# Optimization experiments

Hardware: AMD Instinct MI355X
Metric: run time of the kernel (lower is better)

## Reference

```python
import jax, jax.numpy as jnp
import numpy as np

EPSILON = 1e-8
K = 3  # three-nearest-neighbor interpolation


def setup_inputs() -> dict:
    key = jax.random.key(0)
    k1, k2, k3 = jax.random.split(key, 3)
    B, N1, N2, C = 8, 1024, 4096, 256
    p1 = jax.random.normal(k1, (B, N1, 3), dtype=jnp.float32)  # coarse coords
    x1 = jax.random.normal(k2, (B, C, N1), dtype=jnp.float32)  # coarse features (channel-first)
    p2 = jax.random.normal(k3, (B, N2, 3), dtype=jnp.float32)  # fine coords
    return {"p1": p1, "x1": x1, "p2": p2}


def reference(p1, x1, p2):
    # Squared pairwise distances [B, N2, N1] via the expansion trick.
    d2 = (
        jnp.sum(p2 * p2, axis=-1, keepdims=True)
        - 2.0 * jnp.einsum("bmd,bnd->bmn", p2, p1)
        + jnp.sum(p1 * p1, axis=-1)[:, None, :]
    )
    # K smallest distances (pointops.nearestneighbor returns squared dists).
    neg_top, idx = jax.lax.top_k(-d2, K)  # [B, N2, K]
    dist = -neg_top
    # Reciprocal-distance weights, normalized over the K neighbors.
    dist_recip = 1.0 / (dist + EPSILON)
    weight = dist_recip / jnp.sum(dist_recip, axis=-1, keepdims=True)  # [B, N2, K]
    # Gather neighbor features and blend: up_x1[b,c,m] = sum_k w[b,m,k] * x1[b,c,idx[b,m,k]]
    x1t = jnp.swapaxes(x1, 1, 2)  # [B, N1, C]
    gathered = jax.vmap(lambda f, i: f[i])(x1t, idx)  # [B, N2, K, C]
    up_x1 = jnp.einsum("bmkc,bmk->bcm", gathered, weight)  # [B, C, N2]
    return up_x1
```

## Files before the change

### kernel.cpp

```cpp
#include <hip/hip_runtime.h>
#include <cfloat>
#include <climits>

#define B_   8
#define N1_  1024
#define N2_  4096
#define C_   256
#define TPQ  16
#define QPB  (256 / TPQ)

__device__ __forceinline__ unsigned umin_(unsigned a, unsigned b) { return a < b ? a : b; }

__device__ __forceinline__ unsigned umed3_(unsigned a, unsigned b, unsigned c) {
    unsigned d;
    asm("v_med3_u32 %0, %1, %2, %3" : "=v"(d) : "v"(a), "v"(b), "v"(c));
    return d;
}

#define KINS4(k, k0, k1, k2, k3) do {                 \
    unsigned _n1 = umed3_((k), k0, k1);               \
    unsigned _n2 = umed3_((k), k1, k2);               \
    unsigned _n3 = umed3_((k), k2, k3);               \
    k0 = umin_((k), k0);  k1 = _n1;  k2 = _n2;  k3 = _n3; \
} while (0)

__global__ __launch_bounds__(256) void knn_kernel(
    const float* __restrict__ p1, const float* __restrict__ p2,
    int4* __restrict__ wsi, float4* __restrict__ wsw) {
    __shared__ float4 pts[N1_];

    const int tid   = threadIdx.x;
    const int b     = blockIdx.x >> 8;
    const int mtile = blockIdx.x & 255;

    for (int j = tid; j < N1_; j += 256) {
        float x = p1[((size_t)b * N1_ + j) * 3 + 0];
        float y = p1[((size_t)b * N1_ + j) * 3 + 1];
        float z = p1[((size_t)b * N1_ + j) * 3 + 2];
        float s1 = __fadd_rn(__fadd_rn(__fmul_rn(x, x), __fmul_rn(y, y)),
                             __fmul_rn(z, z));
        pts[j] = make_float4(x + x, y + y, z + z, s1);
    }
    __syncthreads();

    const int q = tid >> 4;
    const int t = tid & 15;
    const int m = mtile * QPB + q;

    const size_t pbase = ((size_t)b * N2_ + m) * 3;
    const float x2 = p2[pbase + 0];
    const float y2 = p2[pbase + 1];
    const float z2 = p2[pbase + 2];
    const float s2 = __fadd_rn(__fadd_rn(__fmul_rn(x2, x2), __fmul_rn(y2, y2)),
                               __fmul_rn(z2, z2));

    unsigned k0 = UINT_MAX, k1 = UINT_MAX, k2 = UINT_MAX, k3 = UINT_MAX;

#pragma unroll 4
    for (int n = t; n < N1_; n += TPQ) {
        float4 p = pts[n];
        float dot2 = __fadd_rn(__fadd_rn(__fmul_rn(x2, p.x), __fmul_rn(y2, p.y)),
                               __fmul_rn(z2, p.z));
        float dd = __fadd_rn(__fsub_rn(s2, dot2), p.w);
        unsigned key = (__float_as_uint(fmaxf(dd, 0.f)) & 0xFFFFFC00u)
                       | (unsigned)n;
        KINS4(key, k0, k1, k2, k3);
    }

    for (int mask = 1; mask < TPQ; mask <<= 1) {
        unsigned p0 = (unsigned)__shfl_xor((int)k0, mask, TPQ);
        unsigned p1_ = (unsigned)__shfl_xor((int)k1, mask, TPQ);
        unsigned p2_ = (unsigned)__shfl_xor((int)k2, mask, TPQ);
        unsigned p3_ = (unsigned)__shfl_xor((int)k3, mask, TPQ);
        KINS4(p0,  k0, k1, k2, k3);
        KINS4(p1_, k0, k1, k2, k3);
        KINS4(p2_, k0, k1, k2, k3);
        KINS4(p3_, k0, k1, k2, k3);
    }

    if (t == 0) {
        int   ix[4];
        float dx[4];
#pragma unroll
        for (int k = 0; k < 4; ++k) {
            const unsigned a = k == 0 ? k0 : k == 1 ? k1 : k == 2 ? k2 : k3;
            const int n = (int)(a & 1023u);
            const float4 c = pts[n];
            dx[k] = __fadd_rn(__fsub_rn(s2,
                __fadd_rn(__fadd_rn(__fmul_rn(x2, c.x), __fmul_rn(y2, c.y)),
                          __fmul_rn(z2, c.z))), c.w);
            ix[k] = n;
        }
#define CSWAP(a, b) do {                                            \
        bool sw = (dx[b] < dx[a]) || (dx[b] == dx[a] && ix[b] < ix[a]); \
        float td = sw ? dx[b] : dx[a]; dx[b] = sw ? dx[a] : dx[b]; dx[a] = td; \
        int   ti = sw ? ix[b] : ix[a]; ix[b] = sw ? ix[a] : ix[b]; ix[a] = ti; \
    } while (0)
        CSWAP(0, 1); CSWAP(2, 3); CSWAP(0, 2); CSWAP(1, 3); CSWAP(1, 2);
#undef CSWAP

        const float r0 = 1.0f / __fadd_rn(dx[0], 1e-8f);
        const float r1 = 1.0f / __fadd_rn(dx[1], 1e-8f);
        const float r2 = 1.0f / __fadd_rn(dx[2], 1e-8f);
        const float s  = __fadd_rn(__fadd_rn(r0, r1), r2);
        const size_t o = (size_t)b * N2_ + m;
        wsi[o] = make_int4(ix[0], ix[1], ix[2], 0);
        wsw[o] = make_float4(r0 / s, r1 / s, r2 / s, 0.0f);
    }
}


__global__ __launch_bounds__(256) void blend_kernel(
    const float* __restrict__ x1, const int4* __restrict__ wsi,
    const float4* __restrict__ wsw, float* __restrict__ out) {
    __shared__ float4 L4[N1_];

    int bid = blockIdx.x;
    const int mhalf = bid & 1;
    const int ct    = (bid >> 1) & 63;
    const int b     = bid >> 7;
    const int tid   = threadIdx.x;

    const size_t wbase = (size_t)b * N2_ + (size_t)mhalf * 2048;
    int4   id[8];
    float4 w[8];
#pragma unroll
    for (int mb = 0; mb < 8; ++mb) {
        id[mb] = wsi[wbase + mb * 256 + tid];
        w[mb]  = wsw[wbase + mb * 256 + tid];
    }

    const float* src = x1 + ((size_t)b * C_ + (size_t)ct * 4) * N1_;
    float4 v[4];
#pragma unroll
    for (int c = 0; c < 4; ++c)
        v[c] = reinterpret_cast<const float4*>(src + (size_t)c * N1_)[tid];
#pragma unroll
    for (int e = 0; e < 4; ++e) {
        const int n = 4 * tid + e;
        L4[n ^ ((n >> 3) & 7)] = make_float4((&v[0].x)[e], (&v[1].x)[e],
                                             (&v[2].x)[e], (&v[3].x)[e]);
    }
    __syncthreads();

    const size_t obase = ((size_t)b * C_ + (size_t)ct * 4) * N2_;
#pragma unroll
    for (int mb = 0; mb < 8; ++mb) {
        const int m = mhalf * 2048 + mb * 256 + tid;
        const int na = id[mb].x, nb = id[mb].y, nc = id[mb].z;
        const float4 A  = L4[na ^ ((na >> 3) & 7)];
        const float4 Bv = L4[nb ^ ((nb >> 3) & 7)];
        const float4 Cv = L4[nc ^ ((nc >> 3) & 7)];
        const float wx = w[mb].x, wy = w[mb].y, wz = w[mb].z;
#pragma unroll
        for (int r = 0; r < 4; ++r) {
            float acc = __fadd_rn(__fadd_rn(__fmul_rn((&A.x)[r],  wx),
                                            __fmul_rn((&Bv.x)[r], wy)),
                                  __fmul_rn((&Cv.x)[r], wz));
            __builtin_nontemporal_store(acc, &out[obase + (size_t)r * N2_ + m]);
        }
    }
}

extern "C" void kernel_launch(void* const* d_in, const int* in_sizes, int n_in,
                              void* d_out, int out_size, void* d_ws, size_t ws_size,
                              hipStream_t stream) {
    const float* p1 = (const float*)d_in[0];
    const float* x1 = (const float*)d_in[1];
    const float* p2 = (const float*)d_in[2];
    float* out = (float*)d_out;

    int4*   wsi = (int4*)d_ws;
    float4* wsw = (float4*)((char*)d_ws + (size_t)B_ * N2_ * sizeof(int4));

    knn_kernel<<<B_ * (N2_ / QPB), 256, 0, stream>>>(p1, p2, wsi, wsw);
    blend_kernel<<<B_ * (C_ / 4) * 2, 256, 0, stream>>>(x1, wsi, wsw, out);
}
```

Before: 32.01 us.

## Sort coarse points by radius and prune KNN search with norm bound

Adds a prep kernel that sorts each batch's coarse points by norm using a shared-memory bitonic sort and stores them in a paired SoA layout. The KNN kernel binary-searches the query norm and expands outward in 32-point chunks. It stops a side once the triangle-inequality bound (|q|-|p|)^2 exceeds the current 3rd-best distance, and it evaluates two points per step with packed float2 math. This is meant to skip most of the 1024 distance evaluations per query, at the cost of an extra kernel launch, a serial bitonic sort on only 8 blocks, and per-iteration shuffle reductions. For Gaussian 3D data the radius shells are wide, so pruning may be weak.

```diff
diff --git a/kernel.cpp b/kernel.cpp
--- a/kernel.cpp
+++ b/kernel.cpp
@@ -9,6 +9,8 @@
 #define TPQ  16
 #define QPB  (256 / TPQ)
 
+typedef float vf2 __attribute__((ext_vector_type(2)));
+
 __device__ __forceinline__ unsigned umin_(unsigned a, unsigned b) { return a < b ? a : b; }
 
 __device__ __forceinline__ unsigned umed3_(unsigned a, unsigned b, unsigned c) {
@@ -24,22 +26,80 @@
     k0 = umin_((k), k0);  k1 = _n1;  k2 = _n2;  k3 = _n3; \
 } while (0)
 
+__global__ __launch_bounds__(256) void prep_kernel(
+    const float* __restrict__ p1, float4* __restrict__ SQ,
+    float4* __restrict__ SR, float* __restrict__ RHO, int* __restrict__ OIDX) {
+    __shared__ unsigned long long key[N1_];
+    __shared__ float sx[N1_], sy[N1_], sz[N1_], ss[N1_];
+
+    const int b   = blockIdx.x;
+    const int tid = threadIdx.x;
+
+    for (int i = tid; i < N1_; i += 256) {
+        float x = p1[((size_t)b * N1_ + i) * 3 + 0];
+        float y = p1[((size_t)b * N1_ + i) * 3 + 1];
+        float z = p1[((size_t)b * N1_ + i) * 3 + 2];
+        float s1 = __fadd_rn(__fadd_rn(__fmul_rn(x, x), __fmul_rn(y, y)),
+                             __fmul_rn(z, z));
+        float rho = sqrtf(s1);
+        key[i] = ((unsigned long long)__float_as_uint(rho) << 32) | (unsigned)i;
+        sx[i] = x; sy[i] = y; sz[i] = z; ss[i] = s1;
+    }
+    __syncthreads();
+
+    for (int k = 2; k <= N1_; k <<= 1) {
+        for (int j = k >> 1; j > 0; j >>= 1) {
+            for (int i = tid; i < N1_; i += 256) {
+                int partner = i ^ j;
+                if (partner > i) {
+                    bool asc = (i & k) == 0;
+                    unsigned long long a = key[i], c = key[partner];
+                    if ((a > c) == asc) { key[i] = c; key[partner] = a; }
+                }
+            }
+            __syncthreads();
+        }
+    }
+
+    for (int s = tid; s < N1_; s += 256) {
+        unsigned long long kk = key[s];
+        RHO[b * N1_ + s]  = __uint_as_float((unsigned)(kk >> 32));
+        OIDX[b * N1_ + s] = (int)(kk & 1023u);
+    }
+    for (int k2 = tid; k2 < N1_ / 2; k2 += 256) {
+        int na = (int)(key[2 * k2] & 1023u);
+        int nb = (int)(key[2 * k2 + 1] & 1023u);
+        float xa = sx[na], ya = sy[na], za = sz[na], sa = ss[na];
+        float xb = sx[nb], yb = sy[nb], zb = sz[nb], sb = ss[nb];
+        SQ[b * (N1_ / 2) + k2] = make_float4(xa + xa, xb + xb, ya + ya, yb + yb);
+        SR[b * (N1_ / 2) + k2] = make_float4(za + za, zb + zb, sa, sb);
+    }
+}
+
 __global__ __launch_bounds__(256) void knn_kernel(
-    const float* __restrict__ p1, const float* __restrict__ p2,
-    int4* __restrict__ wsi, float4* __restrict__ wsw) {
-    __shared__ float4 pts[N1_];
+    const float4* __restrict__ SQ, const float4* __restrict__ SR,
+    const float* __restrict__ RHO, const int* __restrict__ OIDX,
+    const float* __restrict__ p2, int4* __restrict__ wsi,
+    float4* __restrict__ wsw) {
+#pragma clang fp contract(off)
+    __shared__ float4 Q[N1_ / 2];
+    __shared__ float4 R[N1_ / 2];
+    __shared__ float  RH[N1_];
+    __shared__ int    OI[N1_];
 
     const int tid   = threadIdx.x;
     const int b     = blockIdx.x >> 8;
     const int mtile = blockIdx.x & 255;
 
-    for (int j = tid; j < N1_; j += 256) {
-        float x = p1[((size_t)b * N1_ + j) * 3 + 0];
-        float y = p1[((size_t)b * N1_ + j) * 3 + 1];
-        float z = p1[((size_t)b * N1_ + j) * 3 + 2];
-        float s1 = __fadd_rn(__fadd_rn(__fmul_rn(x, x), __fmul_rn(y, y)),
-                             __fmul_rn(z, z));
-        pts[j] = make_float4(x + x, y + y, z + z, s1);
+#pragma unroll
+    for (int i = 0; i < 2; ++i) {
+        Q[tid + 256 * i] = SQ[b * (N1_ / 2) + tid + 256 * i];
+        R[tid + 256 * i] = SR[b * (N1_ / 2) + tid + 256 * i];
+    }
+#pragma unroll
+    for (int i = 0; i < 4; ++i) {
+        RH[tid + 256 * i] = RHO[b * N1_ + tid + 256 * i];
+        OI[tid + 256 * i] = OIDX[b * N1_ + tid + 256 * i];
     }
     __syncthreads();
 
@@ -53,19 +113,81 @@
     const float z2 = p2[pbase + 2];
     const float s2 = __fadd_rn(__fadd_rn(__fmul_rn(x2, x2), __fmul_rn(y2, y2)),
                                __fmul_rn(z2, z2));
+    const float qn = sqrtf(s2);
+
+    const vf2 x2v = {x2, x2};
+    const vf2 y2v = {y2, y2};
+    const vf2 z2v = {z2, z2};
+    const vf2 s2v = {s2, s2};
+
+    int blo = 0, bhi = N1_;
+#pragma unroll
+    for (int it = 0; it < 10; ++it) {
+        int mid = (blo + bhi) >> 1;
+        if (RH[mid] < qn) blo = mid + 1; else bhi = mid;
+    }
+    const int sAligned = blo & ~31;
+    int loBase = sAligned - 32;
+    int hiBase = sAligned;
+    bool doneLo = false, doneHi = false;
 
     unsigned k0 = UINT_MAX, k1 = UINT_MAX, k2 = UINT_MAX, k3 = UINT_MAX;
 
-#pragma unroll 4
-    for (int n = t; n < N1_; n += TPQ) {
-        float4 p = pts[n];
-        float dot2 = __fadd_rn(__fadd_rn(__fmul_rn(x2, p.x), __fmul_rn(y2, p.y)),
-                               __fmul_rn(z2, p.z));
-        float dd = __fadd_rn(__fsub_rn(s2, dot2), p.w);
-        unsigned key = (__float_as_uint(fmaxf(dd, 0.f)) & 0xFFFFFC00u)
-                       | (unsigned)n;
-        KINS4(key, k0, k1, k2, k3);
-    }
+#define EVAL_PAIR(baseSlot, CHECK_NEG) do {                                   \
+    const int pi_ = ((baseSlot) >> 1) + t;                                    \
+    const int pc_ = pi_ < 0 ? 0 : pi_;                                        \
+    float4 qv = Q[pc_]; float4 rv = R[pc_];                                   \
+    vf2 qx = {qv.x, qv.y}, qy = {qv.z, qv.w};                                 \
+    vf2 rz = {rv.x, rv.y}, rs = {rv.z, rv.w};                                 \
+    vf2 t1 = qx * x2v, t2 = qy * y2v, t3 = rz * z2v;                          \
+    vf2 dot2 = (t1 + t2) + t3;                                                \
+    vf2 dd = (s2v - dot2) + rs;                                               \
+    const int s0_ = (baseSlot) + 2 * t;                                       \
+    unsigned ka = (__float_as_uint(fmaxf(dd.x, 0.f)) & 0xFFFFFC00u)           \
+                  | ((unsigned)s0_ & 1023u);                                  \
+    unsigned kb = (__float_as_uint(fmaxf(dd.y, 0.f)) & 0xFFFFFC00u)           \
+                  | (((unsigned)s0_ + 1u) & 1023u);                           \
+    if (CHECK_NEG && s0_ < 0) { ka = 0xFFFFFFFFu; kb = 0xFFFFFFFFu; }         \
+    KINS4(ka, k0, k1, k2, k3);                                                \
+    KINS4(kb, k0, k1, k2, k3);                                                \
+} while (0)
+
+    for (int it = 0; it < 34; ++it) {
+        unsigned k3m = k3;
+        k3m = umin_(k3m, (unsigned)__shfl_xor((int)k3m, 1, TPQ));
+        k3m = umin_(k3m, (unsigned)__shfl_xor((int)k3m, 2, TPQ));
+        k3m = umin_(k3m, (unsigned)__shfl_xor((int)k3m, 4, TPQ));
+        k3m = umin_(k3m, (unsigned)__shfl_xor((int)k3m, 8, TPQ));
+        const unsigned long long kcmp =
+            (unsigned long long)(k3m & 0xFFFFFC00u) + 2048ull;
+
+        doneLo = doneLo || (loBase + 32 <= 0);
+        if (!doneLo) {
+            const float rf = RH[loBase + 31];
+            if (rf < qn) {
+                const float df = qn - rf;
+                const float bnd = df * df;
+                doneLo = ((unsigned long long)(__float_as_uint(bnd)
+                          & 0xFFFFFC00u) > kcmp);
+            }
+        }
+        if (!doneLo) { EVAL_PAIR(loBase, true); loBase -= 32; }
+
+        doneHi = doneHi || (hiBase >= N1_);
+        if (!doneHi) {
+            const float rf = RH[hiBase];
+            if (rf > qn) {
+                const float df = rf - qn;
+                const float bnd = df * df;
+                doneHi = ((unsigned long long)(__float_as_uint(bnd)
+                          & 0xFFFFFC00u) > kcmp);
+            }
+        }
+        if (!doneHi) { EVAL_PAIR(hiBase, false); hiBase += 32; }
+
+        if (__all(doneLo && doneHi)) break;
+    }
+#undef EVAL_PAIR
 
     for (int mask = 1; mask < TPQ; mask <<= 1) {
         unsigned p0 = (unsigned)__shfl_xor((int)k0, mask, TPQ);
@@ -84,12 +206,17 @@
 #pragma unroll
         for (int k = 0; k < 4; ++k) {
             const unsigned a = k == 0 ? k0 : k == 1 ? k1 : k == 2 ? k2 : k3;
-            const int n = (int)(a & 1023u);
-            const float4 c = pts[n];
+            const int slot = (int)(a & 1023u);
+            const int kk = slot >> 1;
+            const int h  = slot & 1;
+            const float cx = h ? Q[kk].y : Q[kk].x;
+            const float cy = h ? Q[kk].w : Q[kk].z;
+            const float cz = h ? R[kk].y : R[kk].x;
+            const float cs = h ? R[kk].w : R[kk].z;
             dx[k] = __fadd_rn(__fsub_rn(s2,
-                __fadd_rn(__fadd_rn(__fmul_rn(x2, c.x), __fmul_rn(y2, c.y)),
-                          __fmul_rn(z2, c.z))), c.w);
-            ix[k] = n;
+                __fadd_rn(__fadd_rn(__fmul_rn(x2, cx), __fmul_rn(y2, cy)),
+                          __fmul_rn(z2, cz))), cs);
+            ix[k] = OI[slot];
         }
 #define CSWAP(a, b) do {                                            \
         bool sw = (dx[b] < dx[a]) || (dx[b] == dx[a] && ix[b] < ix[a]); \
@@ -170,9 +297,16 @@
     const float* p2 = (const float*)d_in[2];
     float* out = (float*)d_out;
 
-    int4*   wsi = (int4*)d_ws;
-    float4* wsw = (float4*)((char*)d_ws + (size_t)B_ * N2_ * sizeof(int4));
-
-    knn_kernel<<<B_ * (N2_ / QPB), 256, 0, stream>>>(p1, p2, wsi, wsw);
+    char* ws = (char*)d_ws;
+    int4*   wsi  = (int4*)ws;
+    float4* wsw  = (float4*)(ws + (size_t)B_ * N2_ * 16);
+    float4* SQ   = (float4*)(ws + (size_t)B_ * N2_ * 32);
+    float4* SR   = (float4*)(ws + (size_t)B_ * N2_ * 32 + 65536);
+    float*  RHO  = (float*) (ws + (size_t)B_ * N2_ * 32 + 131072);
+    int*    OIDX = (int*)   (ws + (size_t)B_ * N2_ * 32 + 163840);
+
+    prep_kernel<<<B_, 256, 0, stream>>>(p1, SQ, SR, RHO, OIDX);
+    knn_kernel<<<B_ * (N2_ / QPB), 256, 0, stream>>>(SQ, SR, RHO, OIDX,
+                                                     p2, wsi, wsw);
     blend_kernel<<<B_ * (C_ / 4) * 2, 256, 0, stream>>>(x1, wsi, wsw, out);
 }
```

Result: slower. 70.24 us (+119.5%).
